# Optimization experiments

Measured on AMD Instinct MI355X. Metric: run time of the kernel, lower is better.

## Reference

```python
import jax, jax.numpy as jnp
import numpy as np

CLARITY_K, CLARITY_SIGMA = 31, 8.0
TEXTURE_K, TEXTURE_SIGMA = 7, 1.5


def _gauss1d(size, sigma):
    grid = np.arange(size, dtype=np.float32) - size // 2
    g = np.exp(-grid ** 2 / (2.0 * sigma * sigma))
    return (g / g.sum()).astype(np.float32)


def _blur(img, g1d):
    # Separable Gaussian blur: the original 2D kernel is the outer product of
    # the normalized 1D gaussian with itself, so two 1D passes are exact.
    size = g1d.shape[0]
    pad = size // 2
    kh = jnp.asarray(g1d, img.dtype).reshape(1, 1, size, 1)  # OIHW, vertical
    kw = jnp.asarray(g1d, img.dtype).reshape(1, 1, 1, size)  # OIHW, horizontal
    dn = jax.lax.conv_dimension_numbers(img.shape, kh.shape, ('NCHW', 'OIHW', 'NCHW'))
    y = jax.lax.conv_general_dilated(img, kh, (1, 1), [(pad, pad), (0, 0)], dimension_numbers=dn)
    y = jax.lax.conv_general_dilated(y, kw, (1, 1), [(0, 0), (pad, pad)], dimension_numbers=dn)
    return y


def setup_inputs() -> dict:
    key = jax.random.key(0)
    kx, kc, kt = jax.random.split(key, 3)
    x = jax.random.uniform(kx, (8, 3, 1024, 1024), dtype=jnp.float32)
    clarity = jax.random.normal(kc, (), dtype=jnp.float32)
    texture = jax.random.normal(kt, (), dtype=jnp.float32)
    return {"x": x, "clarity": clarity, "texture": texture}


def reference(x, clarity, texture):
    g_clar = _gauss1d(CLARITY_K, CLARITY_SIGMA)
    g_tex = _gauss1d(TEXTURE_K, TEXTURE_SIGMA)

    # Rec.709 luma, shape [B,1,H,W]
    luma = 0.2126 * x[:, 0:1] + 0.7152 * x[:, 1:2] + 0.0722 * x[:, 2:3]

    mid_freq = luma - _blur(luma, g_clar)    # 31x31 gaussian
    high_freq = luma - _blur(luma, g_tex)    # 7x7 gaussian

    clarity_amount = jnp.tanh(clarity) * 0.5
    texture_amount = jnp.tanh(texture) * 0.3

    luma_enhanced = luma + clarity_amount * mid_freq + texture_amount * high_freq
    ratio = (luma_enhanced + 1e-6) / (luma + 1e-6)
    return jnp.clip(x * ratio, 0.0, 1.0)
```

## Files before the change

### kernel.cpp

```cpp
#include <hip/hip_runtime.h>
#include <hip/hip_fp16.h>
#include <cmath>

#define HH   1024
#define WW   1024
#define HW   (HH * WW)

#define SW    64
#define TH    128
#define T31R  158
#define T7R   134
#define SPX   112
#define SOFF  24
#define UPR   28

constexpr double cexp(double v) {
    double term = 1.0, sum = 1.0;
    for (int i = 1; i < 64; ++i) { term *= v / (double)i; sum += term; }
    return sum;
}
struct GW { float g31[31]; float g7[7]; };
constexpr GW make_gw() {
    GW r{};
    double t31[31]; double s31 = 0.0;
    for (int i = 0; i < 31; ++i) { double d = (double)(i - 15); t31[i] = cexp(-d * d / 128.0); s31 += t31[i]; }
    for (int i = 0; i < 31; ++i) r.g31[i] = (float)(t31[i] / s31);
    double t7[7]; double s7 = 0.0;
    for (int i = 0; i < 7; ++i) { double d = (double)(i - 3); t7[i] = cexp(-d * d / 4.5); s7 += t7[i]; }
    for (int i = 0; i < 7; ++i) r.g7[i] = (float)(t7[i] / s7);
    return r;
}
__constant__ GW GWC = make_gw();

__global__ __launch_bounds__(256, 4)
void fused_tile(const float* __restrict__ x,
                const float* __restrict__ clar,
                const float* __restrict__ tex,
                float* __restrict__ out) {
    __shared__ __align__(16) __half t31s [T31R][SW];
    __shared__ __align__(16) __half t7s  [T7R][SW];
    __shared__ __align__(16) __half stage[4][4][SPX];

    const int id    = blockIdx.x;
    const int xcd   = id & 7;
    const int k     = id >> 3;
    const int combo = xcd * 16 + (k & 15);
    const int band  = k >> 4;
    const int img   = combo >> 4;
    const int strip = combo & 15;

    const int y0 = band * TH;
    const int x0 = strip * SW;
    const int t  = threadIdx.x;
    const int w    = t >> 6;
    const int lane = t & 63;

    const float* xb = x   + (size_t)img * 3 * HW;
    float*       ob = out + (size_t)img * 3 * HW;

    const int r0s = lane / UPR;
    const int c0s = lane - UPR * r0s;
    const int u1  = lane + 64;
    const bool has1 = (u1 < 4 * UPR);
    const int r1s = u1 / UPR;
    const int c1s = u1 - UPR * r1s;
    const int col0 = x0 - SOFF + 4 * c0s;
    const int col1 = x0 - SOFF + 4 * c1s;
    const bool c0ok = (unsigned)col0 < (unsigned)WW;
    const bool c1ok = (unsigned)col1 < (unsigned)WW;

    float4 R0, G0, B0, R1, G1, B1;

    auto issue = [&](int it) {
        const int gbase = it * 16;
        {
            const int tr = gbase + 4 * w + r0s;
            const int y  = y0 - 15 + tr;
            if (tr < T31R && (unsigned)y < (unsigned)HH && c0ok) {
                const float* xr = xb + (size_t)y * WW + col0;
                R0 = *(const float4*)(xr);
                G0 = *(const float4*)(xr + HW);
                B0 = *(const float4*)(xr + 2 * HW);
            } else {
                R0 = make_float4(0.f, 0.f, 0.f, 0.f); G0 = R0; B0 = R0;
            }
        }
        if (has1) {
            const int tr = gbase + 4 * w + r1s;
            const int y  = y0 - 15 + tr;
            if (tr < T31R && (unsigned)y < (unsigned)HH && c1ok) {
                const float* xr = xb + (size_t)y * WW + col1;
                R1 = *(const float4*)(xr);
                G1 = *(const float4*)(xr + HW);
                B1 = *(const float4*)(xr + 2 * HW);
            } else {
                R1 = make_float4(0.f, 0.f, 0.f, 0.f); G1 = R1; B1 = R1;
            }
        }
    };

    issue(0);

    for (int it = 0; it < 10; ++it) {
        {
            union { float2 f; __half2 h[2]; } W;
            W.h[0] = __floats2half2_rn(fmaf(0.2126f, R0.x, fmaf(0.7152f, G0.x, 0.0722f * B0.x)),
                                       fmaf(0.2126f, R0.y, fmaf(0.7152f, G0.y, 0.0722f * B0.y)));
            W.h[1] = __floats2half2_rn(fmaf(0.2126f, R0.z, fmaf(0.7152f, G0.z, 0.0722f * B0.z)),
                                       fmaf(0.2126f, R0.w, fmaf(0.7152f, G0.w, 0.0722f * B0.w)));
            *(float2*)&stage[w][r0s][4 * c0s] = W.f;
            if (has1) {
                union { float2 f; __half2 h[2]; } V;
                V.h[0] = __floats2half2_rn(fmaf(0.2126f, R1.x, fmaf(0.7152f, G1.x, 0.0722f * B1.x)),
                                           fmaf(0.2126f, R1.y, fmaf(0.7152f, G1.y, 0.0722f * B1.y)));
                V.h[1] = __floats2half2_rn(fmaf(0.2126f, R1.z, fmaf(0.7152f, G1.z, 0.0722f * B1.z)),
                                           fmaf(0.2126f, R1.w, fmaf(0.7152f, G1.w, 0.0722f * B1.w)));
                *(float2*)&stage[w][r1s][4 * c1s] = V.f;
            }
        }

        if (it + 1 < 10) issue(it + 1);

        {
            const int lr = (t >> 4) & 3;
            const int c  = t & 15;
            const int tr = it * 16 + (t >> 4);
            if (tr < T31R) {
                float win[36];
                #pragma unroll
                for (int q = 0; q < 9; ++q) {
                    union { float2 f; __half2 h[2]; } U;
                    U.f = *(const float2*)&stage[w][lr][4 * c + 8 + 4 * q];
                    const float2 a = __half22float2(U.h[0]);
                    const float2 b = __half22float2(U.h[1]);
                    win[4 * q]     = a.x; win[4 * q + 1] = a.y;
                    win[4 * q + 2] = b.x; win[4 * q + 3] = b.y;
                }
                float o[4] = {0.f, 0.f, 0.f, 0.f};
                float p[4] = {0.f, 0.f, 0.f, 0.f};
                #pragma unroll
                for (int s = 0; s < 31; ++s) {
                    const float g = GWC.g31[s];
                    o[0] = fmaf(g, win[1 + s], o[0]);
                    o[1] = fmaf(g, win[2 + s], o[1]);
                    o[2] = fmaf(g, win[3 + s], o[2]);
                    o[3] = fmaf(g, win[4 + s], o[3]);
                }
                #pragma unroll
                for (int s = 0; s < 7; ++s) {
                    const float g = GWC.g7[s];
                    p[0] = fmaf(g, win[13 + s], p[0]);
                    p[1] = fmaf(g, win[14 + s], p[1]);
                    p[2] = fmaf(g, win[15 + s], p[2]);
                    p[3] = fmaf(g, win[16 + s], p[3]);
                }
                union { float2 f; __half2 h[2]; } W;
                W.h[0] = __floats2half2_rn(o[0], o[1]);
                W.h[1] = __floats2half2_rn(o[2], o[3]);
                *(float2*)&t31s[tr][4 * c] = W.f;
                if (tr >= 12 && tr < 12 + T7R) {
                    union { float2 f; __half2 h[2]; } V;
                    V.h[0] = __floats2half2_rn(p[0], p[1]);
                    V.h[1] = __floats2half2_rn(p[2], p[3]);
                    *(float2*)&t7s[tr - 12][4 * c] = V.f;
                }
            }
        }
    }

    __syncthreads();

    const float ca = tanhf(clar[0]) * 0.5f;
    const float ta = tanhf(tex[0]) * 0.3f;

    const int cc = (t & 31) * 2;
    const int rg = t >> 5;
    const int r0 = rg * 16;

    float2 w31[31];
    #pragma unroll
    for (int q = 0; q < 30; ++q)
        w31[q] = __half22float2(*(const __half2*)&t31s[r0 + q][cc]);
    float2 w7[7];
    #pragma unroll
    for (int q = 0; q < 6; ++q)
        w7[q] = __half22float2(*(const __half2*)&t7s[r0 + q][cc]);

    {
    const float* p0 = xb + (size_t)(y0 + r0) * WW + x0 + cc;
    float2 R  = *(const float2*)(p0);
    float2 G  = *(const float2*)(p0 + HW);
    float2 Bc = *(const float2*)(p0 + 2 * HW);

    #pragma unroll
    for (int j = 0; j < 16; ++j) {
        w31[(30 + j) % 31] = __half22float2(*(const __half2*)&t31s[r0 + 30 + j][cc]);
        w7 [(6 + j) % 7]   = __half22float2(*(const __half2*)&t7s [r0 + 6 + j][cc]);

        float2 Rn, Gn, Bn;
        if (j < 15) {
            const float* pn = xb + (size_t)(y0 + r0 + j + 1) * WW + x0 + cc;
            Rn = *(const float2*)(pn);
            Gn = *(const float2*)(pn + HW);
            Bn = *(const float2*)(pn + 2 * HW);
        }

        float2 a31 = make_float2(0.f, 0.f);
        #pragma unroll
        for (int q = 0; q < 31; ++q) {
            const float g = GWC.g31[q];
            const float2 wv = w31[(j + q) % 31];
            a31.x = fmaf(g, wv.x, a31.x);
            a31.y = fmaf(g, wv.y, a31.y);
        }
        float2 a7 = make_float2(0.f, 0.f);
        #pragma unroll
        for (int q = 0; q < 7; ++q) {
            const float g = GWC.g7[q];
            const float2 wv = w7[(j + q) % 7];
            a7.x = fmaf(g, wv.x, a7.x);
            a7.y = fmaf(g, wv.y, a7.y);
        }

        const int y = y0 + r0 + j;
        float* qo = ob + (size_t)y * WW + x0 + cc;

        const float Lx = fmaf(0.2126f, R.x, fmaf(0.7152f, G.x, 0.0722f * Bc.x));
        const float Ly = fmaf(0.2126f, R.y, fmaf(0.7152f, G.y, 0.0722f * Bc.y));
        const float lex = Lx + ca * (Lx - a31.x) + ta * (Lx - a7.x);
        const float ley = Ly + ca * (Ly - a31.y) + ta * (Ly - a7.y);
        const float rx = (lex + 1e-6f) * __builtin_amdgcn_rcpf(Lx + 1e-6f);
        const float ry = (ley + 1e-6f) * __builtin_amdgcn_rcpf(Ly + 1e-6f);

        float2 o0, o1, o2;
        o0.x = fminf(fmaxf(R.x  * rx, 0.f), 1.f);  o0.y = fminf(fmaxf(R.y  * ry, 0.f), 1.f);
        o1.x = fminf(fmaxf(G.x  * rx, 0.f), 1.f);  o1.y = fminf(fmaxf(G.y  * ry, 0.f), 1.f);
        o2.x = fminf(fmaxf(Bc.x * rx, 0.f), 1.f);  o2.y = fminf(fmaxf(Bc.y * ry, 0.f), 1.f);
        *(float2*)(qo)          = o0;
        *(float2*)(qo + HW)     = o1;
        *(float2*)(qo + 2 * HW) = o2;

        if (j < 15) { R = Rn; G = Gn; Bc = Bn; }
    }
    }
}

extern "C" void kernel_launch(void* const* d_in, const int* in_sizes, int n_in,
                              void* d_out, int out_size, void* d_ws, size_t ws_size,
                              hipStream_t stream) {
    const float* x    = (const float*)d_in[0];
    const float* clar = (const float*)d_in[1];
    const float* tex  = (const float*)d_in[2];
    float* out = (float*)d_out;

    dim3 grid(8 * 16 * 8);
    dim3 block(256);
    hipLaunchKernelGGL(fused_tile, grid, block, 0, stream, x, clar, tex, out);
}
```

Before: 199.3 us.

## Shrink staging halo, branchless clamped loads, and restructure vertical pass to float4

Reduces the horizontal staging halo from 112 to 96 pixels so each wave's row fits 24 float4 units, and replaces branchy zero-fill loads with clamped-address loads plus a multiplicative mask, so all loads issue unconditionally. Adds sched_barriers to keep the global prefetch ahead of the horizontal convolution. The vertical pass now has each thread handle 4 columns by 8 rows, reading the blur taps directly from LDS per output row instead of a rolling register window, and uses float4 global loads and stores. This trades more LDS reads for wider memory accesses and lower register pressure.

```diff
diff --git a/kernel.cpp b/kernel.cpp
--- a/kernel.cpp
+++ b/kernel.cpp
@@ -10,9 +10,9 @@
 #define TH    128
 #define T31R  158
 #define T7R   134
-#define SPX   112
-#define SOFF  24
-#define UPR   28
+#define SPX   96
+#define SOFF  16
+#define UPR   24
 
 constexpr double cexp(double v) {
     double term = 1.0, sum = 1.0;
@@ -61,65 +61,66 @@
     const int r0s = lane / UPR;
     const int c0s = lane - UPR * r0s;
     const int u1  = lane + 64;
-    const bool has1 = (u1 < 4 * UPR);
-    const int r1s = u1 / UPR;
-    const int c1s = u1 - UPR * r1s;
+    const int r1r = u1 / UPR;
+    const int r1s = r1r > 3 ? 3 : r1r;
+    const int c1s = u1 - UPR * r1r;
     const int col0 = x0 - SOFF + 4 * c0s;
     const int col1 = x0 - SOFF + 4 * c1s;
-    const bool c0ok = (unsigned)col0 < (unsigned)WW;
-    const bool c1ok = (unsigned)col1 < (unsigned)WW;
+    const int col0c = col0 < 0 ? 0 : (col0 > WW - 4 ? WW - 4 : col0);
+    const int col1c = col1 < 0 ? 0 : (col1 > WW - 4 ? WW - 4 : col1);
+    const float cm0 = ((unsigned)col0 < (unsigned)WW) ? 1.f : 0.f;
+    const float cm1 = ((unsigned)col1 < (unsigned)WW) ? 1.f : 0.f;
 
     float4 R0, G0, B0, R1, G1, B1;
+    float  mk0, mk1;
 
     auto issue = [&](int it) {
         const int gbase = it * 16;
         {
             const int tr = gbase + 4 * w + r0s;
             const int y  = y0 - 15 + tr;
-            if (tr < T31R && (unsigned)y < (unsigned)HH && c0ok) {
-                const float* xr = xb + (size_t)y * WW + col0;
-                R0 = *(const float4*)(xr);
-                G0 = *(const float4*)(xr + HW);
-                B0 = *(const float4*)(xr + 2 * HW);
-            } else {
-                R0 = make_float4(0.f, 0.f, 0.f, 0.f); G0 = R0; B0 = R0;
-            }
-        }
-        if (has1) {
+            const int yc = y < 0 ? 0 : (y > HH - 1 ? HH - 1 : y);
+            mk0 = (tr < T31R && (unsigned)y < (unsigned)HH) ? cm0 : 0.f;
+            const float* xr = xb + (size_t)yc * WW + col0c;
+            R0 = *(const float4*)(xr);
+            G0 = *(const float4*)(xr + HW);
+            B0 = *(const float4*)(xr + 2 * HW);
+        }
+        {
             const int tr = gbase + 4 * w + r1s;
             const int y  = y0 - 15 + tr;
-            if (tr < T31R && (unsigned)y < (unsigned)HH && c1ok) {
-                const float* xr = xb + (size_t)y * WW + col1;
-                R1 = *(const float4*)(xr);
-                G1 = *(const float4*)(xr + HW);
-                B1 = *(const float4*)(xr + 2 * HW);
-            } else {
-                R1 = make_float4(0.f, 0.f, 0.f, 0.f); G1 = R1; B1 = R1;
-            }
+            const int yc = y < 0 ? 0 : (y > HH - 1 ? HH - 1 : y);
+            mk1 = (tr < T31R && (unsigned)y < (unsigned)HH) ? cm1 : 0.f;
+            const float* xr = xb + (size_t)yc * WW + col1c;
+            R1 = *(const float4*)(xr);
+            G1 = *(const float4*)(xr + HW);
+            B1 = *(const float4*)(xr + 2 * HW);
         }
     };
 
     issue(0);
+    __builtin_amdgcn_sched_barrier(0);
 
     for (int it = 0; it < 10; ++it) {
         {
             union { float2 f; __half2 h[2]; } W;
-            W.h[0] = __floats2half2_rn(fmaf(0.2126f, R0.x, fmaf(0.7152f, G0.x, 0.0722f * B0.x)),
-                                       fmaf(0.2126f, R0.y, fmaf(0.7152f, G0.y, 0.0722f * B0.y)));
-            W.h[1] = __floats2half2_rn(fmaf(0.2126f, R0.z, fmaf(0.7152f, G0.z, 0.0722f * B0.z)),
-                                       fmaf(0.2126f, R0.w, fmaf(0.7152f, G0.w, 0.0722f * B0.w)));
+            W.h[0] = __floats2half2_rn(mk0 * fmaf(0.2126f, R0.x, fmaf(0.7152f, G0.x, 0.0722f * B0.x)),
+                                       mk0 * fmaf(0.2126f, R0.y, fmaf(0.7152f, G0.y, 0.0722f * B0.y)));
+            W.h[1] = __floats2half2_rn(mk0 * fmaf(0.2126f, R0.z, fmaf(0.7152f, G0.z, 0.0722f * B0.z)),
+                                       mk0 * fmaf(0.2126f, R0.w, fmaf(0.7152f, G0.w, 0.0722f * B0.w)));
             *(float2*)&stage[w][r0s][4 * c0s] = W.f;
-            if (has1) {
-                union { float2 f; __half2 h[2]; } V;
-                V.h[0] = __floats2half2_rn(fmaf(0.2126f, R1.x, fmaf(0.7152f, G1.x, 0.0722f * B1.x)),
-                                           fmaf(0.2126f, R1.y, fmaf(0.7152f, G1.y, 0.0722f * B1.y)));
-                V.h[1] = __floats2half2_rn(fmaf(0.2126f, R1.z, fmaf(0.7152f, G1.z, 0.0722f * B1.z)),
-                                           fmaf(0.2126f, R1.w, fmaf(0.7152f, G1.w, 0.0722f * B1.w)));
-                *(float2*)&stage[w][r1s][4 * c1s] = V.f;
-            }
-        }
-
-        if (it + 1 < 10) issue(it + 1);
+            union { float2 f; __half2 h[2]; } V;
+            V.h[0] = __floats2half2_rn(mk1 * fmaf(0.2126f, R1.x, fmaf(0.7152f, G1.x, 0.0722f * B1.x)),
+                                       mk1 * fmaf(0.2126f, R1.y, fmaf(0.7152f, G1.y, 0.0722f * B1.y)));
+            V.h[1] = __floats2half2_rn(mk1 * fmaf(0.2126f, R1.z, fmaf(0.7152f, G1.z, 0.0722f * B1.z)),
+                                       mk1 * fmaf(0.2126f, R1.w, fmaf(0.7152f, G1.w, 0.0722f * B1.w)));
+            *(float2*)&stage[w][r1s][4 * c1s] = V.f;
+        }
+
+        if (it + 1 < 10) {
+            issue(it + 1);
+        }
+        __builtin_amdgcn_sched_barrier(0);
 
         {
             const int lr = (t >> 4) & 3;
@@ -130,7 +131,7 @@
                 #pragma unroll
                 for (int q = 0; q < 9; ++q) {
                     union { float2 f; __half2 h[2]; } U;
-                    U.f = *(const float2*)&stage[w][lr][4 * c + 8 + 4 * q];
+                    U.f = *(const float2*)&stage[w][lr][4 * c + 4 * q];
                     const float2 a = __half22float2(U.h[0]);
                     const float2 b = __half22float2(U.h[1]);
                     win[4 * q]     = a.x; win[4 * q + 1] = a.y;
@@ -173,75 +174,89 @@
     const float ca = tanhf(clar[0]) * 0.5f;
     const float ta = tanhf(tex[0]) * 0.3f;
 
-    const int cc = (t & 31) * 2;
-    const int rg = t >> 5;
-    const int r0 = rg * 16;
-
-    float2 w31[31];
+    const int rg = t >> 4;
+    const int r0 = rg * 8;
+    const int cc = 4 * (t & 15);
+
+    const float* p0 = xb + (size_t)(y0 + r0) * WW + x0 + cc;
+    float4 R  = *(const float4*)(p0);
+    float4 G  = *(const float4*)(p0 + HW);
+    float4 Bc = *(const float4*)(p0 + 2 * HW);
+    __builtin_amdgcn_sched_barrier(0);
+
     #pragma unroll
-    for (int q = 0; q < 30; ++q)
-        w31[q] = __half22float2(*(const __half2*)&t31s[r0 + q][cc]);
-    float2 w7[7];
-    #pragma unroll
-    for (int q = 0; q < 6; ++q)
-        w7[q] = __half22float2(*(const __half2*)&t7s[r0 + q][cc]);
-
-    {
-    const float* p0 = xb + (size_t)(y0 + r0) * WW + x0 + cc;
-    float2 R  = *(const float2*)(p0);
-    float2 G  = *(const float2*)(p0 + HW);
-    float2 Bc = *(const float2*)(p0 + 2 * HW);
-
-    #pragma unroll
-    for (int j = 0; j < 16; ++j) {
-        w31[(30 + j) % 31] = __half22float2(*(const __half2*)&t31s[r0 + 30 + j][cc]);
-        w7 [(6 + j) % 7]   = __half22float2(*(const __half2*)&t7s [r0 + 6 + j][cc]);
-
-        float2 Rn, Gn, Bn;
-        if (j < 15) {
+    for (int j = 0; j < 8; ++j) {
+        float4 Rn, Gn, Bn;
+        if (j < 7) {
             const float* pn = xb + (size_t)(y0 + r0 + j + 1) * WW + x0 + cc;
-            Rn = *(const float2*)(pn);
-            Gn = *(const float2*)(pn + HW);
-            Bn = *(const float2*)(pn + 2 * HW);
-        }
-
-        float2 a31 = make_float2(0.f, 0.f);
+            Rn = *(const float4*)(pn);
+            Gn = *(const float4*)(pn + HW);
+            Bn = *(const float4*)(pn + 2 * HW);
+        }
+        __builtin_amdgcn_sched_barrier(0);
+
+        float4 a31 = make_float4(0.f, 0.f, 0.f, 0.f);
         #pragma unroll
         for (int q = 0; q < 31; ++q) {
+            union { float2 f; __half2 h[2]; } U;
+            U.f = *(const float2*)&t31s[r0 + j + q][cc];
+            const float2 a = __half22float2(U.h[0]);
+            const float2 b = __half22float2(U.h[1]);
             const float g = GWC.g31[q];
-            const float2 wv = w31[(j + q) % 31];
-            a31.x = fmaf(g, wv.x, a31.x);
-            a31.y = fmaf(g, wv.y, a31.y);
-        }
-        float2 a7 = make_float2(0.f, 0.f);
+            a31.x = fmaf(g, a.x, a31.x);
+            a31.y = fmaf(g, a.y, a31.y);
+            a31.z = fmaf(g, b.x, a31.z);
+            a31.w = fmaf(g, b.y, a31.w);
+        }
+        float4 a7 = make_float4(0.f, 0.f, 0.f, 0.f);
         #pragma unroll
         for (int q = 0; q < 7; ++q) {
+            union { float2 f; __half2 h[2]; } U;
+            U.f = *(const float2*)&t7s[r0 + j + q][cc];
+            const float2 a = __half22float2(U.h[0]);
+            const float2 b = __half22float2(U.h[1]);
             const float g = GWC.g7[q];
-            const float2 wv = w7[(j + q) % 7];
-            a7.x = fmaf(g, wv.x, a7.x);
-            a7.y = fmaf(g, wv.y, a7.y);
+            a7.x = fmaf(g, a.x, a7.x);
+            a7.y = fmaf(g, a.y, a7.y);
+            a7.z = fmaf(g, b.x, a7.z);
+            a7.w = fmaf(g, b.y, a7.w);
         }
 
         const int y = y0 + r0 + j;
         float* qo = ob + (size_t)y * WW + x0 + cc;
 
-        const float Lx = fmaf(0.2126f, R.x, fmaf(0.7152f, G.x, 0.0722f * Bc.x));
-        const float Ly = fmaf(0.2126f, R.y, fmaf(0.7152f, G.y, 0.0722f * Bc.y));
-        const float lex = Lx + ca * (Lx - a31.x) + ta * (Lx - a7.x);
-        const float ley = Ly + ca * (Ly - a31.y) + ta * (Ly - a7.y);
-        const float rx = (lex + 1e-6f) * __builtin_amdgcn_rcpf(Lx + 1e-6f);
-        const float ry = (ley + 1e-6f) * __builtin_amdgcn_rcpf(Ly + 1e-6f);
-
-        float2 o0, o1, o2;
-        o0.x = fminf(fmaxf(R.x  * rx, 0.f), 1.f);  o0.y = fminf(fmaxf(R.y  * ry, 0.f), 1.f);
-        o1.x = fminf(fmaxf(G.x  * rx, 0.f), 1.f);  o1.y = fminf(fmaxf(G.y  * ry, 0.f), 1.f);
-        o2.x = fminf(fmaxf(Bc.x * rx, 0.f), 1.f);  o2.y = fminf(fmaxf(Bc.y * ry, 0.f), 1.f);
-        *(float2*)(qo)          = o0;
-        *(float2*)(qo + HW)     = o1;
-        *(float2*)(qo + 2 * HW) = o2;
-
-        if (j < 15) { R = Rn; G = Gn; Bc = Bn; }
-    }
+        float4 o0, o1, o2;
+        {
+            const float L0 = fmaf(0.2126f, R.x, fmaf(0.7152f, G.x, 0.0722f * Bc.x));
+            const float L1 = fmaf(0.2126f, R.y, fmaf(0.7152f, G.y, 0.0722f * Bc.y));
+            const float L2 = fmaf(0.2126f, R.z, fmaf(0.7152f, G.z, 0.0722f * Bc.z));
+            const float L3 = fmaf(0.2126f, R.w, fmaf(0.7152f, G.w, 0.0722f * Bc.w));
+            const float e0 = L0 + ca * (L0 - a31.x) + ta * (L0 - a7.x);
+            const float e1 = L1 + ca * (L1 - a31.y) + ta * (L1 - a7.y);
+            const float e2 = L2 + ca * (L2 - a31.z) + ta * (L2 - a7.z);
+            const float e3 = L3 + ca * (L3 - a31.w) + ta * (L3 - a7.w);
+            const float r0r = (e0 + 1e-6f) * __builtin_amdgcn_rcpf(L0 + 1e-6f);
+            const float r1r = (e1 + 1e-6f) * __builtin_amdgcn_rcpf(L1 + 1e-6f);
+            const float r2r = (e2 + 1e-6f) * __builtin_amdgcn_rcpf(L2 + 1e-6f);
+            const float r3r = (e3 + 1e-6f) * __builtin_amdgcn_rcpf(L3 + 1e-6f);
+            o0.x = fminf(fmaxf(R.x  * r0r, 0.f), 1.f);
+            o0.y = fminf(fmaxf(R.y  * r1r, 0.f), 1.f);
+            o0.z = fminf(fmaxf(R.z  * r2r, 0.f), 1.f);
+            o0.w = fminf(fmaxf(R.w  * r3r, 0.f), 1.f);
+            o1.x = fminf(fmaxf(G.x  * r0r, 0.f), 1.f);
+            o1.y = fminf(fmaxf(G.y  * r1r, 0.f), 1.f);
+            o1.z = fminf(fmaxf(G.z  * r2r, 0.f), 1.f);
+            o1.w = fminf(fmaxf(G.w  * r3r, 0.f), 1.f);
+            o2.x = fminf(fmaxf(Bc.x * r0r, 0.f), 1.f);
+            o2.y = fminf(fmaxf(Bc.y * r1r, 0.f), 1.f);
+            o2.z = fminf(fmaxf(Bc.z * r2r, 0.f), 1.f);
+            o2.w = fminf(fmaxf(Bc.w * r3r, 0.f), 1.f);
+        }
+        *(float4*)(qo)          = o0;
+        *(float4*)(qo + HW)     = o1;
+        *(float4*)(qo + 2 * HW) = o2;
+
+        if (j < 7) { R = Rn; G = Gn; Bc = Bn; }
     }
 }
 
```

Measured after the change: 200.4 us. About the same (+0.5%).
